# Kernel tuning notes

Measured on AMD Instinct MI355X. Metric: run time of the kernel, lower is better.

Reference implementation:

```python
import jax, jax.numpy as jnp
import numpy as np
from jax import lax

V_TH = 1.0    # init kwarg 'thresh'
ALPHA = 1.0   # init kwarg 'alpha' (surrogate-gradient width, unused in fwd)

T, B, N = 32, 32, 65536


def setup_inputs() -> dict:
    key = jax.random.key(0)
    x = jax.random.normal(key, (T, B, N), dtype=jnp.float32)
    return {"x": x}


def reference(x) -> jnp.ndarray:
    # Integrate-and-fire neuron, TBN layout, sequential scan over time:
    #   m_t = v_{t-1} + x_t            (integrate)
    #   y_t = heaviside(m_t - v_th)    (fire)
    #   v_t = m_t - y_t * v_th         (soft reset by subtraction)
    def step(v, x_t):
        m = v + x_t
        y = (m >= V_TH).astype(x_t.dtype)
        v_new = m - y * V_TH
        return v_new, y

    v0 = jnp.zeros_like(x[0])
    _, y_seq = lax.scan(step, v0, x)
    return y_seq
```

## Files before the change

### kernel.cpp

```cpp
#include <hip/hip_runtime.h>


typedef float v4f __attribute__((ext_vector_type(4)));

#define T_STEPS 32
#define PF 8

__global__ __launch_bounds__(256, 8) void if_kernel(const v4f* __restrict__ x,
                                                    v4f* __restrict__ y,
                                                    int bn4) {
    int idx = blockIdx.x * blockDim.x + threadIdx.x;
    if (idx >= bn4) return;

    const v4f* xp = x + idx;

    float v0 = 0.f, v1 = 0.f, v2 = 0.f, v3 = 0.f;
    unsigned m0 = 0u, m1 = 0u, m2 = 0u, m3 = 0u;

    v4f r[PF];
#pragma unroll
    for (int j = 0; j < PF; ++j) {
        const v4f* p = xp + (size_t)j * bn4;
        asm volatile("global_load_dwordx4 %0, %1, off"
                     : "=v"(r[j])
                     : "v"(p));
    }

#define IF_STEP(T_, N_)                                                      \
    {                                                                        \
        asm volatile("s_waitcnt vmcnt(" #N_ ")"                              \
                     : "+v"(r[(T_) & (PF - 1)]));                            \
        v4f xv = r[(T_) & (PF - 1)];                                         \
        if ((T_) + PF < T_STEPS) {                                           \
            const v4f* p = xp + (size_t)((T_) + PF) * bn4;                   \
            asm volatile("global_load_dwordx4 %0, %1, off"                   \
                         : "=v"(r[(T_) & (PF - 1)])                          \
                         : "v"(p));                                          \
        }                                                                    \
        float a0 = v0 + xv.x;                                                \
        float a1 = v1 + xv.y;                                                \
        float a2 = v2 + xv.z;                                                \
        float a3 = v3 + xv.w;                                                \
        bool s0 = a0 >= 1.0f;                                                \
        bool s1 = a1 >= 1.0f;                                                \
        bool s2 = a2 >= 1.0f;                                                \
        bool s3 = a3 >= 1.0f;                                                \
        m0 |= (unsigned)s0 << (T_);                                          \
        m1 |= (unsigned)s1 << (T_);                                          \
        m2 |= (unsigned)s2 << (T_);                                          \
        m3 |= (unsigned)s3 << (T_);                                          \
        v0 = s0 ? a0 - 1.0f : a0;                                            \
        v1 = s1 ? a1 - 1.0f : a1;                                            \
        v2 = s2 ? a2 - 1.0f : a2;                                            \
        v3 = s3 ? a3 - 1.0f : a3;                                            \
    }

    IF_STEP(0, 7)  IF_STEP(1, 7)  IF_STEP(2, 7)  IF_STEP(3, 7)
    IF_STEP(4, 7)  IF_STEP(5, 7)  IF_STEP(6, 7)  IF_STEP(7, 7)
    IF_STEP(8, 7)  IF_STEP(9, 7)  IF_STEP(10, 7) IF_STEP(11, 7)
    IF_STEP(12, 7) IF_STEP(13, 7) IF_STEP(14, 7) IF_STEP(15, 7)
    IF_STEP(16, 7) IF_STEP(17, 7) IF_STEP(18, 7) IF_STEP(19, 7)
    IF_STEP(20, 7) IF_STEP(21, 7) IF_STEP(22, 7) IF_STEP(23, 7)
    IF_STEP(24, 7) IF_STEP(25, 6) IF_STEP(26, 5) IF_STEP(27, 4)
    IF_STEP(28, 3) IF_STEP(29, 2) IF_STEP(30, 1) IF_STEP(31, 0)
#undef IF_STEP

    v4f* yp = y + idx;
#pragma unroll
    for (int t = 0; t < T_STEPS; ++t) {
        v4f out;
        out.x = ((m0 >> t) & 1u) ? 1.0f : 0.0f;
        out.y = ((m1 >> t) & 1u) ? 1.0f : 0.0f;
        out.z = ((m2 >> t) & 1u) ? 1.0f : 0.0f;
        out.w = ((m3 >> t) & 1u) ? 1.0f : 0.0f;
        __builtin_nontemporal_store(out, yp + (size_t)t * bn4);
    }
}

extern "C" void kernel_launch(void* const* d_in, const int* in_sizes, int n_in,
                              void* d_out, int out_size, void* d_ws, size_t ws_size,
                              hipStream_t stream) {
    const float* x = (const float*)d_in[0];
    float* y = (float*)d_out;

    int total = in_sizes[0];
    int bn = total / T_STEPS;
    int bn4 = bn / 4;

    int block = 256;
    int grid = (bn4 + block - 1) / block;

    if_kernel<<<grid, block, 0, stream>>>((const v4f*)x, (v4f*)y, bn4);
}
```

Before: 482.2 us.

## Interleave per-step stores with double-buffered chunked prefetch of inputs

Replaces the inline-asm rolling prefetch with two 8-deep register buffers loaded in chunks through plain loads, letting the compiler place the waitcnts. Each output is now written right after its step is computed, instead of packing spikes into bitmasks and storing all 32 steps at the end. This overlaps writes with the scan and spreads the store traffic. The occupancy hint drops from 8 to 4 waves per SIMD to allow the larger register buffers. The risk is lower latency hiding from fewer resident waves, plus less precise control over memory ordering.

```diff
diff --git a/kernel.cpp b/kernel.cpp
--- a/kernel.cpp
+++ b/kernel.cpp
@@ -4,39 +4,29 @@
 typedef float v4f __attribute__((ext_vector_type(4)));
 
 #define T_STEPS 32
-#define PF 8
+#define CH 8
 
-__global__ __launch_bounds__(256, 8) void if_kernel(const v4f* __restrict__ x,
+__global__ __launch_bounds__(256, 4) void if_kernel(const v4f* __restrict__ x,
                                                     v4f* __restrict__ y,
                                                     int bn4) {
     int idx = blockIdx.x * blockDim.x + threadIdx.x;
     if (idx >= bn4) return;
 
     const v4f* xp = x + idx;
+    v4f* yp = y + idx;
 
     float v0 = 0.f, v1 = 0.f, v2 = 0.f, v3 = 0.f;
-    unsigned m0 = 0u, m1 = 0u, m2 = 0u, m3 = 0u;
 
-    v4f r[PF];
-#pragma unroll
-    for (int j = 0; j < PF; ++j) {
-        const v4f* p = xp + (size_t)j * bn4;
-        asm volatile("global_load_dwordx4 %0, %1, off"
-                     : "=v"(r[j])
-                     : "v"(p));
+    v4f A[CH], B[CH];
+
+#define PREFETCH(BUF, TBASE)                                                 \
+    _Pragma("unroll") for (int j = 0; j < CH; ++j) {                         \
+        BUF[j] = xp[(size_t)((TBASE) + j) * bn4];                            \
     }
 
-#define IF_STEP(T_, N_)                                                      \
+#define IF_STEP(BUF, J, T)                                                   \
     {                                                                        \
-        asm volatile("s_waitcnt vmcnt(" #N_ ")"                              \
-                     : "+v"(r[(T_) & (PF - 1)]));                            \
-        v4f xv = r[(T_) & (PF - 1)];                                         \
-        if ((T_) + PF < T_STEPS) {                                           \
-            const v4f* p = xp + (size_t)((T_) + PF) * bn4;                   \
-            asm volatile("global_load_dwordx4 %0, %1, off"                   \
-                         : "=v"(r[(T_) & (PF - 1)])                          \
-                         : "v"(p));                                          \
-        }                                                                    \
+        v4f xv = BUF[J];                                                     \
         float a0 = v0 + xv.x;                                                \
         float a1 = v1 + xv.y;                                                \
         float a2 = v2 + xv.z;                                                \
@@ -45,36 +35,44 @@
         bool s1 = a1 >= 1.0f;                                                \
         bool s2 = a2 >= 1.0f;                                                \
         bool s3 = a3 >= 1.0f;                                                \
-        m0 |= (unsigned)s0 << (T_);                                          \
-        m1 |= (unsigned)s1 << (T_);                                          \
-        m2 |= (unsigned)s2 << (T_);                                          \
-        m3 |= (unsigned)s3 << (T_);                                          \
+        v4f out;                                                             \
+        out.x = s0 ? 1.0f : 0.0f;                                            \
+        out.y = s1 ? 1.0f : 0.0f;                                            \
+        out.z = s2 ? 1.0f : 0.0f;                                            \
+        out.w = s3 ? 1.0f : 0.0f;                                            \
+        __builtin_nontemporal_store(out, yp + (size_t)(T)*bn4);              \
         v0 = s0 ? a0 - 1.0f : a0;                                            \
         v1 = s1 ? a1 - 1.0f : a1;                                            \
         v2 = s2 ? a2 - 1.0f : a2;                                            \
         v3 = s3 ? a3 - 1.0f : a3;                                            \
     }
 
-    IF_STEP(0, 7)  IF_STEP(1, 7)  IF_STEP(2, 7)  IF_STEP(3, 7)
-    IF_STEP(4, 7)  IF_STEP(5, 7)  IF_STEP(6, 7)  IF_STEP(7, 7)
-    IF_STEP(8, 7)  IF_STEP(9, 7)  IF_STEP(10, 7) IF_STEP(11, 7)
-    IF_STEP(12, 7) IF_STEP(13, 7) IF_STEP(14, 7) IF_STEP(15, 7)
-    IF_STEP(16, 7) IF_STEP(17, 7) IF_STEP(18, 7) IF_STEP(19, 7)
-    IF_STEP(20, 7) IF_STEP(21, 7) IF_STEP(22, 7) IF_STEP(23, 7)
-    IF_STEP(24, 7) IF_STEP(25, 6) IF_STEP(26, 5) IF_STEP(27, 4)
-    IF_STEP(28, 3) IF_STEP(29, 2) IF_STEP(30, 1) IF_STEP(31, 0)
+#define PROCESS(BUF, TBASE)                                                  \
+    IF_STEP(BUF, 0, (TBASE) + 0)                                             \
+    IF_STEP(BUF, 1, (TBASE) + 1)                                             \
+    IF_STEP(BUF, 2, (TBASE) + 2)                                             \
+    IF_STEP(BUF, 3, (TBASE) + 3)                                             \
+    IF_STEP(BUF, 4, (TBASE) + 4)                                             \
+    IF_STEP(BUF, 5, (TBASE) + 5)                                             \
+    IF_STEP(BUF, 6, (TBASE) + 6)                                             \
+    IF_STEP(BUF, 7, (TBASE) + 7)
+
+    PREFETCH(A, 0)
+
+    PREFETCH(B, CH)
+    PROCESS(A, 0)
+
+    PREFETCH(A, 2 * CH)
+    PROCESS(B, CH)
+
+    PREFETCH(B, 3 * CH)
+    PROCESS(A, 2 * CH)
+
+    PROCESS(B, 3 * CH)
+
+#undef PROCESS
 #undef IF_STEP
-
-    v4f* yp = y + idx;
-#pragma unroll
-    for (int t = 0; t < T_STEPS; ++t) {
-        v4f out;
-        out.x = ((m0 >> t) & 1u) ? 1.0f : 0.0f;
-        out.y = ((m1 >> t) & 1u) ? 1.0f : 0.0f;
-        out.z = ((m2 >> t) & 1u) ? 1.0f : 0.0f;
-        out.w = ((m3 >> t) & 1u) ? 1.0f : 0.0f;
-        __builtin_nontemporal_store(out, yp + (size_t)t * bn4);
-    }
+#undef PREFETCH
 }
 
 extern "C" void kernel_launch(void* const* d_in, const int* in_sizes, int n_in,
```

After: 485.4 us. About the same (+0.7%).
